# Kernel tuning notes

Measured on AMD Instinct MI355X. Metric: run time of the kernel, lower is better.

The kernel has to match this reference:

```python
import jax, jax.numpy as jnp
import numpy as np

B, L, DIM, HID, WIN = 1, 512, 64, 128, 4


def _ln(x, scale, bias, eps=1e-6):
    m = jnp.mean(x, axis=-1, keepdims=True)
    v = jnp.var(x, axis=-1, keepdims=True)
    return (x - m) / jnp.sqrt(v + eps) * scale + bias


def _banded_ingoing(left, right, w):
    # out[b,i,j,h] = sum_{k=i-w}^{i+w} left[b,k,i,h] * right[b,k,j,h]
    n = left.shape[1]
    ii = jnp.arange(n)
    offs = jnp.arange(-w, w + 1)
    rows = ii[:, None] + offs[None, :]                      # [L, 2w+1]
    valid = ((rows >= 0) & (rows < n)).astype(left.dtype)
    rows_c = jnp.clip(rows, 0, n - 1)
    # Lb[b,i,d,h] = left[b, i+d, i, h] (zero outside range)
    Lb = left[:, rows_c, ii[:, None], :] * valid[None, :, :, None]  # [B,L,2w+1,H]
    out = jnp.zeros_like(right)
    for di, dd in enumerate(range(-w, w + 1)):
        if dd >= 0:
            sh = jnp.pad(right[:, dd:], ((0, 0), (0, dd), (0, 0), (0, 0)))
        else:
            sh = jnp.pad(right[:, :dd], ((0, 0), (-dd, 0), (0, 0), (0, 0)))
        out = out + Lb[:, :, di, None, :] * sh
    return out


def setup_inputs() -> dict:
    key = jax.random.key(0)
    ks = jax.random.split(key, 8)
    d = {}
    d["x"] = jax.random.normal(ks[0], (B, L, L, DIM), dtype=jnp.float32)
    d["src_mask"] = jnp.ones((B, L), dtype=jnp.int32)
    d["norm_scale"] = jnp.ones((DIM,), jnp.float32)
    d["norm_bias"] = jnp.zeros((DIM,), jnp.float32)
    for i, nm in enumerate(["l", "r", "lg", "rg", "og"]):
        d[f"W{nm}"] = jax.random.normal(ks[i + 1], (DIM, HID), jnp.float32) * 0.02
        d[f"b{nm}"] = jnp.zeros((HID,), jnp.float32)
    d["out_norm_scale"] = jnp.ones((HID,), jnp.float32)
    d["out_norm_bias"] = jnp.zeros((HID,), jnp.float32)
    d["Wo"] = jax.random.normal(ks[6], (HID, DIM), jnp.float32) * 0.02
    d["bo"] = jnp.zeros((DIM,), jnp.float32)
    return d


def reference(x, src_mask, norm_scale, norm_bias, Wl, bl, Wr, br, Wlg, blg,
              Wrg, brg, Wog, bog, out_norm_scale, out_norm_bias, Wo, bo):
    m = src_mask.astype(jnp.float32)
    mask = (m[:, :, None] * m[:, None, :])[..., None]        # [B,L,L,1]
    xn = _ln(x, norm_scale, norm_bias)
    left = (xn @ Wl + bl) * mask * jax.nn.sigmoid(xn @ Wlg + blg)
    right = (xn @ Wr + br) * mask * jax.nn.sigmoid(xn @ Wrg + brg)
    out_gate = jax.nn.sigmoid(xn @ Wog + bog)
    out = _banded_ingoing(left, right, WIN)
    out = _ln(out, out_norm_scale, out_norm_bias) * out_gate
    return out @ Wo + bo
```

## Files before the change

### kernel.cpp

```cpp
#include <hip/hip_runtime.h>

typedef unsigned short u16;
typedef unsigned int u32;

#define LL 512
#define DIMC 64
#define HIDC 128

typedef __attribute__((ext_vector_type(8))) __bf16 bf16x8;
typedef __attribute__((ext_vector_type(4))) float f32x4;

__device__ __forceinline__ u16 f2bf(float f) {
  u32 u = __float_as_uint(f);
  u = u + 0x7FFFu + ((u >> 16) & 1u);
  return (u16)(u >> 16);
}
__device__ __forceinline__ float bf2f(u32 us) {
  return __uint_as_float(us << 16);
}
__device__ __forceinline__ float sigm(float x) {
  return 1.0f / (1.0f + __expf(-x));
}

extern "C" __global__ void prep(const float* __restrict__ Wr, const float* __restrict__ Wrg,
                                const float* __restrict__ Wog, const float* __restrict__ Wl,
                                const float* __restrict__ Wlg, const float* __restrict__ Wo,
                                u16* __restrict__ WTr, u16* __restrict__ WTl,
                                u16* __restrict__ WoT)
{
  int t = blockIdx.x * blockDim.x + threadIdx.x;
  int stride = gridDim.x * blockDim.x;
  for (int idx = t; idx < 384 * 64; idx += stride) {
    int n = idx >> 6, k = idx & 63;
    const float* W = (n < 128) ? Wr : (n < 256 ? Wrg : Wog);
    WTr[(n << 6) + (((k >> 3) ^ (n & 7)) << 3) + (k & 7)] = f2bf(W[k * HIDC + (n & 127)]);
  }
  for (int idx = t; idx < 256 * 64; idx += stride) {
    int n = idx >> 6, k = idx & 63;
    const float* W = (n < 128) ? Wl : Wlg;
    WTl[(n << 6) + (((k >> 3) ^ (n & 7)) << 3) + (k & 7)] = f2bf(W[k * HIDC + (n & 127)]);
  }
  for (int idx = t; idx < 64 * 128; idx += stride) {
    int d = idx >> 7, k = idx & 127;
    WoT[(d << 7) + (((k >> 3) ^ (d & 7)) << 3) + (k & 7)] = f2bf(Wo[k * DIMC + d]);
  }
}

extern "C" __global__ void __launch_bounds__(256, 2)
kernA(const float* __restrict__ x, const int* __restrict__ smask,
      const float* __restrict__ ns, const float* __restrict__ nb,
      const float* __restrict__ br, const float* __restrict__ brg,
      const float* __restrict__ bog, const u16* __restrict__ WTr,
      u16* __restrict__ ring, u16* og, int k0, int i0, int chunk)
{
  __shared__ u16 sWT[384 * 64];
  __shared__ u16 sA[64 * 64];
  __shared__ u16 sR[64 * 136];
  const int bid = blockIdx.x;
  const int slot = bid >> 3, tile = bid & 7;
  const int p = k0 + slot;
  if (p < 0 || p >= LL) return;
  const bool store_og = (p >= i0) && (p < i0 + chunk);
  const int t = threadIdx.x;
  const int lane = t & 63;
  const int wave = t >> 6;
  const int l15 = lane & 15, l4 = lane >> 4;
  const int q0 = tile * 64;

  {
    const uint4* src = (const uint4*)WTr;
    uint4* dst = (uint4*)sWT;
#pragma unroll
    for (int c = 0; c < 12; ++c) dst[t + c * 256] = src[t + c * 256];
  }

  const float mrow = (float)smask[p];
  const int ql = t >> 2, qc = t & 3;
  float4 nsv[4], nbv[4];
#pragma unroll
  for (int j = 0; j < 4; j++) {
    nsv[j] = *(const float4*)(ns + qc * 16 + j * 4);
    nbv[j] = *(const float4*)(nb + qc * 16 + j * 4);
  }
  float brv[2], brgv[2], bogv[2];
#pragma unroll
  for (int fp = 0; fp < 2; fp++) {
    int h = wave * 32 + fp * 16 + l15;
    brv[fp] = br[h]; brgv[fp] = brg[h]; bogv[fp] = bog[h];
  }

  {
    const int q = q0 + ql;
    const float* xp = x + ((size_t)p * LL + q) * DIMC + qc * 16;
    float4 xv[4];
    float s = 0.f, ss = 0.f;
#pragma unroll
    for (int j = 0; j < 4; j++) {
      xv[j] = *(const float4*)(xp + j * 4);
      s += xv[j].x + xv[j].y + xv[j].z + xv[j].w;
      ss += xv[j].x * xv[j].x + xv[j].y * xv[j].y + xv[j].z * xv[j].z + xv[j].w * xv[j].w;
    }
    s += __shfl_xor(s, 1); ss += __shfl_xor(ss, 1);
    s += __shfl_xor(s, 2); ss += __shfl_xor(ss, 2);
    const float mean = s * (1.f / 64.f);
    const float var = ss * (1.f / 64.f) - mean * mean;
    const float rstd = rsqrtf(var + 1e-6f);
    u16 xb[16];
#pragma unroll
    for (int j = 0; j < 4; j++) {
      xb[j*4+0] = f2bf((xv[j].x - mean) * rstd * nsv[j].x + nbv[j].x);
      xb[j*4+1] = f2bf((xv[j].y - mean) * rstd * nsv[j].y + nbv[j].y);
      xb[j*4+2] = f2bf((xv[j].z - mean) * rstd * nsv[j].z + nbv[j].z);
      xb[j*4+3] = f2bf((xv[j].w - mean) * rstd * nsv[j].w + nbv[j].w);
    }
    uint4 c0, c1;
    c0.x = (u32)xb[0]  | ((u32)xb[1]  << 16);
    c0.y = (u32)xb[2]  | ((u32)xb[3]  << 16);
    c0.z = (u32)xb[4]  | ((u32)xb[5]  << 16);
    c0.w = (u32)xb[6]  | ((u32)xb[7]  << 16);
    c1.x = (u32)xb[8]  | ((u32)xb[9]  << 16);
    c1.y = (u32)xb[10] | ((u32)xb[11] << 16);
    c1.z = (u32)xb[12] | ((u32)xb[13] << 16);
    c1.w = (u32)xb[14] | ((u32)xb[15] << 16);
    char* rowp = (char*)sA + ql * 128;
    *(uint4*)(rowp + (((qc * 2 + 0) ^ (ql & 7)) << 4)) = c0;
    *(uint4*)(rowp + (((qc * 2 + 1) ^ (ql & 7)) << 4)) = c1;
  }
  __syncthreads();
  f32x4 acc[4][6];
  f32x4 zero = {0.f, 0.f, 0.f, 0.f};
#pragma unroll
  for (int m = 0; m < 4; m++)
#pragma unroll
    for (int f = 0; f < 6; f++) acc[m][f] = zero;
#pragma unroll
  for (int ks = 0; ks < 2; ks++) {
    bf16x8 av[4];
#pragma unroll
    for (int m = 0; m < 4; m++) {
      int row = m * 16 + l15;
      int ch = (ks * 4 + l4) ^ (row & 7);
      av[m] = *(const bf16x8*)((const char*)sA + row * 128 + (ch << 4));
    }
#pragma unroll
    for (int f = 0; f < 6; f++) {
      int g = f >> 1, fp = f & 1;
      int n = g * 128 + wave * 32 + fp * 16 + l15;
      int ch = (ks * 4 + l4) ^ (n & 7);
      bf16x8 bv = *(const bf16x8*)((const char*)sWT + n * 128 + (ch << 4));
#pragma unroll
      for (int m = 0; m < 4; m++)
        acc[m][f] = __builtin_amdgcn_mfma_f32_16x16x32_bf16(av[m], bv, acc[m][f], 0, 0, 0);
    }
  }
  float mv[4];
#pragma unroll
  for (int r = 0; r < 4; r++)
    mv[r] = mrow;
#pragma unroll
  for (int m = 0; m < 4; m++) {
    float mvr[4];
#pragma unroll
    for (int r = 0; r < 4; r++)
      mvr[r] = mrow * (float)smask[q0 + m * 16 + l4 * 4 + r];
#pragma unroll
    for (int fp = 0; fp < 2; fp++) {
      const int h = wave * 32 + fp * 16 + l15;
      f32x4 lin = acc[m][fp];
      f32x4 gat = acc[m][2 + fp];
#pragma unroll
      for (int r = 0; r < 4; r++) {
        const int row = m * 16 + l4 * 4 + r;
        sR[row * 136 + h] = f2bf((lin[r] + brv[fp]) * mvr[r] * sigm(gat[r] + brgv[fp]));
      }
    }
  }
  __syncthreads();
  {
    uint4* dst = (uint4*)(ring + ((size_t)slot * LL + q0) * HIDC);
#pragma unroll
    for (int c = 0; c < 4; c++) {
      const int g = t + c * 256;
      dst[g] = *(const uint4*)(sR + (g >> 4) * 136 + (g & 15) * 8);
    }
  }
  if (store_og) {
    __syncthreads();
#pragma unroll
    for (int m = 0; m < 4; m++)
#pragma unroll
      for (int fp = 0; fp < 2; fp++) {
        const int h = wave * 32 + fp * 16 + l15;
        f32x4 ogv = acc[m][4 + fp];
#pragma unroll
        for (int r = 0; r < 4; r++) {
          const int row = m * 16 + l4 * 4 + r;
          sR[row * 136 + h] = f2bf(sigm(ogv[r] + bogv[fp]));
        }
      }
    __syncthreads();
    uint4* dst = (uint4*)(og + ((size_t)p * LL + q0) * HIDC);
#pragma unroll
    for (int c = 0; c < 4; c++) {
      const int g = t + c * 256;
      dst[g] = *(const uint4*)(sR + (g >> 4) * 136 + (g & 15) * 8);
    }
  }
}

extern "C" __global__ void __launch_bounds__(256, 2)
kernL(const float* __restrict__ x, const int* __restrict__ smask,
      const float* __restrict__ ns, const float* __restrict__ nb,
      const float* __restrict__ bl, const float* __restrict__ blg,
      const u16* __restrict__ WTl, float* __restrict__ Lbuf)
{
  __shared__ u16 sW[256 * 64];
  __shared__ u16 sA[64 * 64];
  const int g0 = blockIdx.x * 64;
  const int t = threadIdx.x;
  const int lane = t & 63, wave = t >> 6;
  const int l15 = lane & 15, l4 = lane >> 4;

  {
    const uint4* src = (const uint4*)WTl;
    uint4* dst = (uint4*)sW;
#pragma unroll
    for (int c = 0; c < 8; ++c) dst[t + c * 256] = src[t + c * 256];
  }

  const int ql = t >> 2, qc = t & 3;
  {
    const int g = g0 + ql;
    const int i = g / 9, d = g - 9 * i;
    int p = i + d - 4;
    p = (p < 0) ? 0 : (p > LL - 1 ? LL - 1 : p);
    const float* xp = x + ((size_t)p * LL + i) * DIMC + qc * 16;
    float4 xv[4];
    float s = 0.f, ss = 0.f;
#pragma unroll
    for (int j = 0; j < 4; j++) {
      xv[j] = *(const float4*)(xp + j * 4);
      s += xv[j].x + xv[j].y + xv[j].z + xv[j].w;
      ss += xv[j].x * xv[j].x + xv[j].y * xv[j].y + xv[j].z * xv[j].z + xv[j].w * xv[j].w;
    }
    s += __shfl_xor(s, 1); ss += __shfl_xor(ss, 1);
    s += __shfl_xor(s, 2); ss += __shfl_xor(ss, 2);
    const float mean = s * (1.f / 64.f);
    const float rstd = rsqrtf(ss * (1.f / 64.f) - mean * mean + 1e-6f);
    u16 xb[16];
#pragma unroll
    for (int j = 0; j < 4; j++) {
      const float4 nsv = *(const float4*)(ns + qc * 16 + j * 4);
      const float4 nbv = *(const float4*)(nb + qc * 16 + j * 4);
      xb[j*4+0] = f2bf((xv[j].x - mean) * rstd * nsv.x + nbv.x);
      xb[j*4+1] = f2bf((xv[j].y - mean) * rstd * nsv.y + nbv.y);
      xb[j*4+2] = f2bf((xv[j].z - mean) * rstd * nsv.z + nbv.z);
      xb[j*4+3] = f2bf((xv[j].w - mean) * rstd * nsv.w + nbv.w);
    }
    uint4 c0, c1;
    c0.x = (u32)xb[0]  | ((u32)xb[1]  << 16);
    c0.y = (u32)xb[2]  | ((u32)xb[3]  << 16);
    c0.z = (u32)xb[4]  | ((u32)xb[5]  << 16);
    c0.w = (u32)xb[6]  | ((u32)xb[7]  << 16);
    c1.x = (u32)xb[8]  | ((u32)xb[9]  << 16);
    c1.y = (u32)xb[10] | ((u32)xb[11] << 16);
    c1.z = (u32)xb[12] | ((u32)xb[13] << 16);
    c1.w = (u32)xb[14] | ((u32)xb[15] << 16);
    char* rowp = (char*)sA + ql * 128;
    *(uint4*)(rowp + (((qc * 2 + 0) ^ (ql & 7)) << 4)) = c0;
    *(uint4*)(rowp + (((qc * 2 + 1) ^ (ql & 7)) << 4)) = c1;
  }
  __syncthreads();
  f32x4 acc[4][4];
  f32x4 zero = {0.f, 0.f, 0.f, 0.f};
#pragma unroll
  for (int m = 0; m < 4; m++)
#pragma unroll
    for (int f = 0; f < 4; f++) acc[m][f] = zero;
#pragma unroll
  for (int ks = 0; ks < 2; ks++) {
    bf16x8 av[4];
#pragma unroll
    for (int m = 0; m < 4; m++) {
      int row = m * 16 + l15;
      int ch = (ks * 4 + l4) ^ (row & 7);
      av[m] = *(const bf16x8*)((const char*)sA + row * 128 + (ch << 4));
    }
#pragma unroll
    for (int f = 0; f < 4; f++) {
      int grp = f >> 1, fp = f & 1;
      int n = grp * 128 + wave * 32 + fp * 16 + l15;
      int ch = (ks * 4 + l4) ^ (n & 7);
      bf16x8 bv = *(const bf16x8*)((const char*)sW + n * 128 + (ch << 4));
#pragma unroll
      for (int m = 0; m < 4; m++)
        acc[m][f] = __builtin_amdgcn_mfma_f32_16x16x32_bf16(av[m], bv, acc[m][f], 0, 0, 0);
    }
  }
#pragma unroll
  for (int fp = 0; fp < 2; fp++) {
    const int h = wave * 32 + fp * 16 + l15;
    const float blv = bl[h], blgv = blg[h];
#pragma unroll
    for (int m = 0; m < 4; m++) {
      f32x4 lin = acc[m][fp];
      f32x4 gat = acc[m][2 + fp];
#pragma unroll
      for (int r = 0; r < 4; r++) {
        const int g = g0 + m * 16 + l4 * 4 + r;
        const int i = g / 9, d = g - 9 * i;
        const int p = i + d - 4;
        const bool valid = (p >= 0) && (p < LL);
        const float mv = valid ? (float)smask[i] * (float)smask[valid ? p : 0] : 0.f;
        Lbuf[(size_t)g * HIDC + h] = (lin[r] + blv) * mv * sigm(gat[r] + blgv);
      }
    }
  }
}

extern "C" __global__ void __launch_bounds__(256, 4)
kernB(const u16* __restrict__ ring, const u16* og,
      const float* __restrict__ Lbuf, const u16* __restrict__ WoT,
      const float* __restrict__ osc, const float* __restrict__ obi,
      const float* __restrict__ bo, float* out, int k0, int i0)
{
  __shared__ u16 sWo[64 * 128];
  __shared__ u16 sA[64 * 128];
  __shared__ float sLb[9 * 128];
  const int bid = blockIdx.x;
  const int i = i0 + (bid >> 3), j0 = (bid & 7) * 64;
  const int t = threadIdx.x;
  const int lane = t & 63, wave = t >> 6;
  const int l15 = lane & 15, l4 = lane >> 4;
  {
    const uint4* src = (const uint4*)WoT;
    uint4* dst = (uint4*)sWo;
#pragma unroll
    for (int c = 0; c < 4; ++c) dst[t + c * 256] = src[t + c * 256];
    const float* lb = Lbuf + (size_t)i * (9 * HIDC);
    for (int idx = t; idx < 9 * HIDC; idx += 256) sLb[idx] = lb[idx];
  }
  __syncthreads();
  const int j = t >> 2, hq = t & 3, h0 = hq * 32;
  float acc[32];
#pragma unroll
  for (int e = 0; e < 32; e++) acc[e] = 0.f;
  for (int d = 0; d < 9; d++) {
    const int k = i + d - 4;
    if (k < 0 || k >= LL) continue;
    const int slot = k - k0;
    const u16* rp = ring + ((size_t)slot * LL + j0 + j) * HIDC + h0;
#pragma unroll
    for (int c4 = 0; c4 < 4; c4++) {
      uint4 rv = *(const uint4*)(rp + c4 * 8);
      const float4 lb0 = *(const float4*)(sLb + d * 128 + h0 + c4 * 8);
      const float4 lb1 = *(const float4*)(sLb + d * 128 + h0 + c4 * 8 + 4);
      acc[c4*8+0] = fmaf(lb0.x, bf2f(rv.x & 0xffff), acc[c4*8+0]);
      acc[c4*8+1] = fmaf(lb0.y, bf2f(rv.x >> 16),    acc[c4*8+1]);
      acc[c4*8+2] = fmaf(lb0.z, bf2f(rv.y & 0xffff), acc[c4*8+2]);
      acc[c4*8+3] = fmaf(lb0.w, bf2f(rv.y >> 16),    acc[c4*8+3]);
      acc[c4*8+4] = fmaf(lb1.x, bf2f(rv.z & 0xffff), acc[c4*8+4]);
      acc[c4*8+5] = fmaf(lb1.y, bf2f(rv.z >> 16),    acc[c4*8+5]);
      acc[c4*8+6] = fmaf(lb1.z, bf2f(rv.w & 0xffff), acc[c4*8+6]);
      acc[c4*8+7] = fmaf(lb1.w, bf2f(rv.w >> 16),    acc[c4*8+7]);
    }
  }
  float s = 0.f, ss = 0.f;
#pragma unroll
  for (int e = 0; e < 32; e++) { s += acc[e]; ss += acc[e] * acc[e]; }
  s += __shfl_xor(s, 1); ss += __shfl_xor(ss, 1);
  s += __shfl_xor(s, 2); ss += __shfl_xor(ss, 2);
  const float mean = s * (1.f / 128.f);
  const float rstd = rsqrtf(ss * (1.f / 128.f) - mean * mean + 1e-6f);
  const u16* ogp = og + ((size_t)i * LL + j0 + j) * HIDC + h0;
  char* rowp = (char*)sA + j * 256;
#pragma unroll
  for (int c4 = 0; c4 < 4; c4++) {
    const float4 o0 = *(const float4*)(osc + h0 + c4 * 8);
    const float4 o1 = *(const float4*)(osc + h0 + c4 * 8 + 4);
    const float4 b0 = *(const float4*)(obi + h0 + c4 * 8);
    const float4 b1 = *(const float4*)(obi + h0 + c4 * 8 + 4);
    uint4 gv = *(const uint4*)(ogp + c4 * 8);
    float v0 = ((acc[c4*8+0] - mean) * rstd * o0.x + b0.x) * bf2f(gv.x & 0xffff);
    float v1 = ((acc[c4*8+1] - mean) * rstd * o0.y + b0.y) * bf2f(gv.x >> 16);
    float v2 = ((acc[c4*8+2] - mean) * rstd * o0.z + b0.z) * bf2f(gv.y & 0xffff);
    float v3 = ((acc[c4*8+3] - mean) * rstd * o0.w + b0.w) * bf2f(gv.y >> 16);
    float v4 = ((acc[c4*8+4] - mean) * rstd * o1.x + b1.x) * bf2f(gv.z & 0xffff);
    float v5 = ((acc[c4*8+5] - mean) * rstd * o1.y + b1.y) * bf2f(gv.z >> 16);
    float v6 = ((acc[c4*8+6] - mean) * rstd * o1.z + b1.z) * bf2f(gv.w & 0xffff);
    float v7 = ((acc[c4*8+7] - mean) * rstd * o1.w + b1.w) * bf2f(gv.w >> 16);
    uint4 pk;
    pk.x = (u32)f2bf(v0) | ((u32)f2bf(v1) << 16);
    pk.y = (u32)f2bf(v2) | ((u32)f2bf(v3) << 16);
    pk.z = (u32)f2bf(v4) | ((u32)f2bf(v5) << 16);
    pk.w = (u32)f2bf(v6) | ((u32)f2bf(v7) << 16);
    *(uint4*)(rowp + (((hq * 4 + c4) ^ (j & 7)) << 4)) = pk;
  }
  __syncthreads();
  f32x4 acc2[4];
  f32x4 zero = {0.f, 0.f, 0.f, 0.f};
#pragma unroll
  for (int m = 0; m < 4; m++) acc2[m] = zero;
#pragma unroll
  for (int ks = 0; ks < 4; ks++) {
    int n = wave * 16 + l15;
    int chb = (ks * 4 + l4) ^ (n & 7);
    bf16x8 bv = *(const bf16x8*)((const char*)sWo + n * 256 + (chb << 4));
#pragma unroll
    for (int m = 0; m < 4; m++) {
      int row = m * 16 + l15;
      int cha = (ks * 4 + l4) ^ (row & 7);
      bf16x8 av = *(const bf16x8*)((const char*)sA + row * 256 + (cha << 4));
      acc2[m] = __builtin_amdgcn_mfma_f32_16x16x32_bf16(av, bv, acc2[m], 0, 0, 0);
    }
  }
  const int dim = wave * 16 + l15;
  const float bov = bo[dim];
#pragma unroll
  for (int m = 0; m < 4; m++) {
#pragma unroll
    for (int r = 0; r < 4; r++) {
      int jj = j0 + m * 16 + l4 * 4 + r;
      out[((size_t)i * LL + jj) * DIMC + dim] = acc2[m][r] + bov;
    }
  }
}

extern "C" void kernel_launch(void* const* d_in, const int* in_sizes, int n_in,
                              void* d_out, int out_size, void* d_ws, size_t ws_size,
                              hipStream_t stream) {
  const float* x    = (const float*)d_in[0];
  const int*   sm   = (const int*)d_in[1];
  const float* ns   = (const float*)d_in[2];
  const float* nb   = (const float*)d_in[3];
  const float* Wl   = (const float*)d_in[4];
  const float* bl   = (const float*)d_in[5];
  const float* Wr   = (const float*)d_in[6];
  const float* br   = (const float*)d_in[7];
  const float* Wlg  = (const float*)d_in[8];
  const float* blg  = (const float*)d_in[9];
  const float* Wrg  = (const float*)d_in[10];
  const float* brg  = (const float*)d_in[11];
  const float* Wog  = (const float*)d_in[12];
  const float* bog  = (const float*)d_in[13];
  const float* osc  = (const float*)d_in[14];
  const float* obi  = (const float*)d_in[15];
  const float* Wo   = (const float*)d_in[16];
  const float* bo   = (const float*)d_in[17];

  const size_t LBUF_BYTES = (size_t)LL * 9 * HIDC * 4;
  char* ws = (char*)d_ws;
  float* Lbuf = (float*)ws;
  u16* WTr = (u16*)(ws + LBUF_BYTES);
  u16* WTl = (u16*)(ws + LBUF_BYTES + 49152);
  u16* WoT = (u16*)(ws + LBUF_BYTES + 49152 + 32768);
  u16* ring = (u16*)(ws + LBUF_BYTES + 49152 + 32768 + 16384);

  int CHUNK = 256;
  if (ws_size < LBUF_BYTES + 98304 + (size_t)(256 + 8) * LL * HIDC * 2) CHUNK = 64;
  u16* ogB = (u16*)d_out;

  prep<<<32, 256, 0, stream>>>(Wr, Wrg, Wog, Wl, Wlg, Wo, WTr, WTl, WoT);
  kernL<<<72, 256, 0, stream>>>(x, sm, ns, nb, bl, blg, WTl, Lbuf);
  for (int i0 = 0; i0 < LL; i0 += CHUNK) {
    const int k0 = i0 - 4;
    kernA<<<(CHUNK + 8) * 8, 256, 0, stream>>>(x, sm, ns, nb, br, brg, bog,
                                               WTr, ring, ogB, k0, i0, CHUNK);
    kernB<<<CHUNK * 8, 256, 0, stream>>>(ring, ogB, Lbuf, WoT, osc, obi, bo,
                                         (float*)d_out, k0, i0);
  }
}
```

Before: 175.7 us.

## Split right-projection kernel into separate ring and out-gate kernels

Splits the fused right/gate/out-gate projection kernel into two kernels. One computes only the gated right projection into the ring buffer, with less shared memory and fewer accumulators, so it can run with a higher occupancy bound. The other recomputes LayerNorm of x and produces only the out-gate. The staging through shared memory for coalesced stores is removed in favor of direct scattered 2-byte global writes. The split adds an extra launch per chunk and re-reads and re-normalizes x for the out-gate.

```diff
diff --git a/kernel.cpp b/kernel.cpp
--- a/kernel.cpp
+++ b/kernel.cpp
@@ -21,6 +21,7 @@
 __device__ __forceinline__ float sigm(float x) {
   return 1.0f / (1.0f + __expf(-x));
 }
+
 
 extern "C" __global__ void prep(const float* __restrict__ Wr, const float* __restrict__ Wrg,
                                 const float* __restrict__ Wog, const float* __restrict__ Wl,
@@ -46,21 +47,18 @@
   }
 }
 
-extern "C" __global__ void __launch_bounds__(256, 2)
-kernA(const float* __restrict__ x, const int* __restrict__ smask,
-      const float* __restrict__ ns, const float* __restrict__ nb,
-      const float* __restrict__ br, const float* __restrict__ brg,
-      const float* __restrict__ bog, const u16* __restrict__ WTr,
-      u16* __restrict__ ring, u16* og, int k0, int i0, int chunk)
+extern "C" __global__ void __launch_bounds__(256, 3)
+kernRing(const float* __restrict__ x, const int* __restrict__ smask,
+         const float* __restrict__ ns, const float* __restrict__ nb,
+         const float* __restrict__ br, const float* __restrict__ brg,
+         const u16* __restrict__ WTr, u16* __restrict__ ring, int k0)
 {
-  __shared__ u16 sWT[384 * 64];
+  __shared__ u16 sWT[256 * 64];
   __shared__ u16 sA[64 * 64];
-  __shared__ u16 sR[64 * 136];
   const int bid = blockIdx.x;
   const int slot = bid >> 3, tile = bid & 7;
   const int p = k0 + slot;
   if (p < 0 || p >= LL) return;
-  const bool store_og = (p >= i0) && (p < i0 + chunk);
   const int t = threadIdx.x;
   const int lane = t & 63;
   const int wave = t >> 6;
@@ -71,7 +69,7 @@
     const uint4* src = (const uint4*)WTr;
     uint4* dst = (uint4*)sWT;
 #pragma unroll
-    for (int c = 0; c < 12; ++c) dst[t + c * 256] = src[t + c * 256];
+    for (int c = 0; c < 8; ++c) dst[t + c * 256] = src[t + c * 256];
   }
 
   const float mrow = (float)smask[p];
@@ -82,11 +80,11 @@
     nsv[j] = *(const float4*)(ns + qc * 16 + j * 4);
     nbv[j] = *(const float4*)(nb + qc * 16 + j * 4);
   }
-  float brv[2], brgv[2], bogv[2];
+  float brv[2], brgv[2];
 #pragma unroll
   for (int fp = 0; fp < 2; fp++) {
     int h = wave * 32 + fp * 16 + l15;
-    brv[fp] = br[h]; brgv[fp] = brg[h]; bogv[fp] = bog[h];
+    brv[fp] = br[h]; brgv[fp] = brg[h];
   }
 
   {
@@ -127,12 +125,12 @@
     *(uint4*)(rowp + (((qc * 2 + 1) ^ (ql & 7)) << 4)) = c1;
   }
   __syncthreads();
-  f32x4 acc[4][6];
+  f32x4 acc[4][4];
   f32x4 zero = {0.f, 0.f, 0.f, 0.f};
 #pragma unroll
   for (int m = 0; m < 4; m++)
 #pragma unroll
-    for (int f = 0; f < 6; f++) acc[m][f] = zero;
+    for (int f = 0; f < 4; f++) acc[m][f] = zero;
 #pragma unroll
   for (int ks = 0; ks < 2; ks++) {
     bf16x8 av[4];
@@ -143,7 +141,7 @@
       av[m] = *(const bf16x8*)((const char*)sA + row * 128 + (ch << 4));
     }
 #pragma unroll
-    for (int f = 0; f < 6; f++) {
+    for (int f = 0; f < 4; f++) {
       int g = f >> 1, fp = f & 1;
       int n = g * 128 + wave * 32 + fp * 16 + l15;
       int ch = (ks * 4 + l4) ^ (n & 7);
@@ -153,10 +151,6 @@
         acc[m][f] = __builtin_amdgcn_mfma_f32_16x16x32_bf16(av[m], bv, acc[m][f], 0, 0, 0);
     }
   }
-  float mv[4];
-#pragma unroll
-  for (int r = 0; r < 4; r++)
-    mv[r] = mrow;
 #pragma unroll
   for (int m = 0; m < 4; m++) {
     float mvr[4];
@@ -170,42 +164,121 @@
       f32x4 gat = acc[m][2 + fp];
 #pragma unroll
       for (int r = 0; r < 4; r++) {
-        const int row = m * 16 + l4 * 4 + r;
-        sR[row * 136 + h] = f2bf((lin[r] + brv[fp]) * mvr[r] * sigm(gat[r] + brgv[fp]));
+        const int qq = q0 + m * 16 + l4 * 4 + r;
+        ring[((size_t)slot * LL + qq) * HIDC + h] =
+            f2bf((lin[r] + brv[fp]) * mvr[r] * sigm(gat[r] + brgv[fp]));
       }
     }
   }
+}
+
+extern "C" __global__ void __launch_bounds__(256, 4)
+kernOg(const float* __restrict__ x, const int* __restrict__ smask,
+       const float* __restrict__ ns, const float* __restrict__ nb,
+       const float* __restrict__ bog, const u16* __restrict__ WTr,
+       u16* __restrict__ og, int i0)
+{
+  __shared__ u16 sWog[128 * 64];
+  __shared__ u16 sA[64 * 64];
+  const int bid = blockIdx.x;
+  const int p = i0 + (bid >> 3);
+  const int tile = bid & 7;
+  const int t = threadIdx.x;
+  const int lane = t & 63;
+  const int wave = t >> 6;
+  const int l15 = lane & 15, l4 = lane >> 4;
+  const int q0 = tile * 64;
+
+  {
+    const uint4* src = (const uint4*)(WTr + 256 * 64);
+    uint4* dst = (uint4*)sWog;
+#pragma unroll
+    for (int c = 0; c < 4; ++c) dst[t + c * 256] = src[t + c * 256];
+  }
+
+  const int ql = t >> 2, qc = t & 3;
+  float4 nsv[4], nbv[4];
+#pragma unroll
+  for (int j = 0; j < 4; j++) {
+    nsv[j] = *(const float4*)(ns + qc * 16 + j * 4);
+    nbv[j] = *(const float4*)(nb + qc * 16 + j * 4);
+  }
+  float bogv[2];
+#pragma unroll
+  for (int fp = 0; fp < 2; fp++) bogv[fp] = bog[wave * 32 + fp * 16 + l15];
+
+  {
+    const int q = q0 + ql;
+    const float* xp = x + ((size_t)p * LL + q) * DIMC + qc * 16;
+    float4 xv[4];
+    float s = 0.f, ss = 0.f;
+#pragma unroll
+    for (int j = 0; j < 4; j++) {
+      xv[j] = *(const float4*)(xp + j * 4);
+      s += xv[j].x + xv[j].y + xv[j].z + xv[j].w;
+      ss += xv[j].x * xv[j].x + xv[j].y * xv[j].y + xv[j].z * xv[j].z + xv[j].w * xv[j].w;
+    }
+    s += __shfl_xor(s, 1); ss += __shfl_xor(ss, 1);
+    s += __shfl_xor(s, 2); ss += __shfl_xor(ss, 2);
+    const float mean = s * (1.f / 64.f);
+    const float rstd = rsqrtf(ss * (1.f / 64.f) - mean * mean + 1e-6f);
+    u16 xb[16];
+#pragma unroll
+    for (int j = 0; j < 4; j++) {
+      xb[j*4+0] = f2bf((xv[j].x - mean) * rstd * nsv[j].x + nbv[j].x);
+      xb[j*4+1] = f2bf((xv[j].y - mean) * rstd * nsv[j].y + nbv[j].y);
+      xb[j*4+2] = f2bf((xv[j].z - mean) * rstd * nsv[j].z + nbv[j].z);
+      xb[j*4+3] = f2bf((xv[j].w - mean) * rstd * nsv[j].w + nbv[j].w);
+    }
+    uint4 c0, c1;
+    c0.x = (u32)xb[0]  | ((u32)xb[1]  << 16);
+    c0.y = (u32)xb[2]  | ((u32)xb[3]  << 16);
+    c0.z = (u32)xb[4]  | ((u32)xb[5]  << 16);
+    c0.w = (u32)xb[6]  | ((u32)xb[7]  << 16);
+    c1.x = (u32)xb[8]  | ((u32)xb[9]  << 16);
+    c1.y = (u32)xb[10] | ((u32)xb[11] << 16);
+    c1.z = (u32)xb[12] | ((u32)xb[13] << 16);
+    c1.w = (u32)xb[14] | ((u32)xb[15] << 16);
+    char* rowp = (char*)sA + ql * 128;
+    *(uint4*)(rowp + (((qc * 2 + 0) ^ (ql & 7)) << 4)) = c0;
+    *(uint4*)(rowp + (((qc * 2 + 1) ^ (ql & 7)) << 4)) = c1;
+  }
   __syncthreads();
-  {
-    uint4* dst = (uint4*)(ring + ((size_t)slot * LL + q0) * HIDC);
-#pragma unroll
-    for (int c = 0; c < 4; c++) {
-      const int g = t + c * 256;
-      dst[g] = *(const uint4*)(sR + (g >> 4) * 136 + (g & 15) * 8);
-    }
-  }
-  if (store_og) {
-    __syncthreads();
-#pragma unroll
-    for (int m = 0; m < 4; m++)
-#pragma unroll
-      for (int fp = 0; fp < 2; fp++) {
-        const int h = wave * 32 + fp * 16 + l15;
-        f32x4 ogv = acc[m][4 + fp];
-#pragma unroll
-        for (int r = 0; r < 4; r++) {
-          const int row = m * 16 + l4 * 4 + r;
-          sR[row * 136 + h] = f2bf(sigm(ogv[r] + bogv[fp]));
-        }
+  f32x4 acc[4][2];
+  f32x4 zero = {0.f, 0.f, 0.f, 0.f};
+#pragma unroll
+  for (int m = 0; m < 4; m++) { acc[m][0] = zero; acc[m][1] = zero; }
+#pragma unroll
+  for (int ks = 0; ks < 2; ks++) {
+    bf16x8 av[4];
+#pragma unroll
+    for (int m = 0; m < 4; m++) {
+      int row = m * 16 + l15;
+      int ch = (ks * 4 + l4) ^ (row & 7);
+      av[m] = *(const bf16x8*)((const char*)sA + row * 128 + (ch << 4));
+    }
+#pragma unroll
+    for (int fp = 0; fp < 2; fp++) {
+      int n = wave * 32 + fp * 16 + l15;
+      int ch = (ks * 4 + l4) ^ (n & 7);
+      bf16x8 bv = *(const bf16x8*)((const char*)sWog + n * 128 + (ch << 4));
+#pragma unroll
+      for (int m = 0; m < 4; m++)
+        acc[m][fp] = __builtin_amdgcn_mfma_f32_16x16x32_bf16(av[m], bv, acc[m][fp], 0, 0, 0);
+    }
+  }
+#pragma unroll
+  for (int m = 0; m < 4; m++)
+#pragma unroll
+    for (int fp = 0; fp < 2; fp++) {
+      const int h = wave * 32 + fp * 16 + l15;
+      f32x4 ogv = acc[m][fp];
+#pragma unroll
+      for (int r = 0; r < 4; r++) {
+        const int qq = q0 + m * 16 + l4 * 4 + r;
+        og[((size_t)p * LL + qq) * HIDC + h] = f2bf(sigm(ogv[r] + bogv[fp]));
       }
-    __syncthreads();
-    uint4* dst = (uint4*)(og + ((size_t)p * LL + q0) * HIDC);
-#pragma unroll
-    for (int c = 0; c < 4; c++) {
-      const int g = t + c * 256;
-      dst[g] = *(const uint4*)(sR + (g >> 4) * 136 + (g & 15) * 8);
-    }
-  }
+    }
 }
 
 extern "C" __global__ void __launch_bounds__(256, 2)
@@ -464,8 +537,8 @@
   kernL<<<72, 256, 0, stream>>>(x, sm, ns, nb, bl, blg, WTl, Lbuf);
   for (int i0 = 0; i0 < LL; i0 += CHUNK) {
     const int k0 = i0 - 4;
-    kernA<<<(CHUNK + 8) * 8, 256, 0, stream>>>(x, sm, ns, nb, br, brg, bog,
-                                               WTr, ring, ogB, k0, i0, CHUNK);
+    kernRing<<<(CHUNK + 8) * 8, 256, 0, stream>>>(x, sm, ns, nb, br, brg, WTr, ring, k0);
+    kernOg<<<CHUNK * 8, 256, 0, stream>>>(x, sm, ns, nb, bog, WTr, ogB, i0);
     kernB<<<CHUNK * 8, 256, 0, stream>>>(ring, ogB, Lbuf, WoT, osc, obi, bo,
                                          (float*)d_out, k0, i0);
   }
```

After: 183.3 us. +4.3%, slower.
